# Kernel optimization log

Hardware: AMD Instinct MI355X
Metric: run time of the kernel (lower is better)

## Reference

```python
import jax, jax.numpy as jnp
import numpy as np

B = 32768
D_A, D_V, D_T = 512, 512, 768
D_KW, D_CTX, D_SPK = 256, 256, 128
H = 512
IN_A = D_V + D_T + D_KW + D_CTX + D_SPK  # 1920 = visual + other_dim (text+hidden+speaker)
IN_V = D_A + D_T + D_KW + D_CTX + D_SPK  # 1920


def _linear_params(key, din, dout):
    kw, kb = jax.random.split(key)
    bound = 1.0 / np.sqrt(din)
    W = jax.random.uniform(kw, (din, dout), jnp.float32, -bound, bound)
    b = jax.random.uniform(kb, (dout,), jnp.float32, -bound, bound)
    return W, b


def setup_inputs() -> dict:
    key = jax.random.key(0)
    ks = jax.random.split(key, 16)
    inp = {
        'audio': jax.random.normal(ks[0], (B, D_A), jnp.float32),
        'visual': jax.random.normal(ks[1], (B, D_V), jnp.float32),
        'text': jax.random.normal(ks[2], (B, D_T), jnp.float32),
        'keywords': jax.random.normal(ks[3], (B, D_KW), jnp.float32),
        'context': jax.random.normal(ks[4], (B, D_CTX), jnp.float32),
        'speaker_embed': jax.random.normal(ks[5], (B, D_SPK), jnp.float32),
    }
    # Masks restricted to dimensionally-consistent patterns: [0,1,1] or [1,0,1]
    r = jax.random.randint(ks[6], (B,), 0, 2)
    inp['modality_masks'] = jnp.stack([r, 1 - r, jnp.ones_like(r)], axis=1).astype(jnp.int32)
    # audio_imagination MLP params
    inp['aW1'], inp['ab1'] = _linear_params(ks[7], IN_A, H)
    inp['aW2'], inp['ab2'] = _linear_params(ks[8], H, H)
    inp['aW3'], inp['ab3'] = _linear_params(ks[9], H, D_A)
    # visual_imagination MLP params
    inp['vW1'], inp['vb1'] = _linear_params(ks[10], IN_V, H)
    inp['vW2'], inp['vb2'] = _linear_params(ks[11], H, H)
    inp['vW3'], inp['vb3'] = _linear_params(ks[12], H, D_V)
    return inp


def _mlp(x, W1, b1, W2, b2, W3, b3):
    h = jax.nn.relu(x @ W1 + b1)  # dropout is eval-mode identity
    h = jax.nn.relu(h @ W2 + b2)
    return h @ W3 + b3


def reference(audio, visual, text, keywords, context, speaker_embed, modality_masks,
              aW1, ab1, aW2, ab2, aW3, ab3,
              vW1, vb1, vW2, vb2, vW3, vb3):
    m = modality_masks.astype(audio.dtype)
    common = jnp.concatenate([keywords, context, speaker_embed], axis=-1)  # [B, 640]
    in_a = jnp.concatenate([visual, text, common], axis=-1)  # [B, IN_A]
    in_v = jnp.concatenate([audio, text, common], axis=-1)   # [B, IN_V]
    # Rows where the modality is present (mask==1) were omitted in the original
    # ragged stacking; here they are zeroed to keep a fixed [B, D] output.
    recon_audio = _mlp(in_a, aW1, ab1, aW2, ab2, aW3, ab3) * (1.0 - m[:, 0:1])
    recon_visual = _mlp(in_v, vW1, vb1, vW2, vb2, vW3, vb3) * (1.0 - m[:, 1:2])
    return recon_audio, recon_visual
```

## Files before the change

kernel.cpp:

```cpp
#include <hip/hip_runtime.h>
#include <stdint.h>

typedef __bf16 bf16;
typedef __bf16 bf16x8 __attribute__((ext_vector_type(8)));
typedef float  f32x4  __attribute__((ext_vector_type(4)));

#define NROWS 32768
#define HID   512
#define PADM  17408

__device__ __forceinline__ void gload_lds16(const void* g, void* l) {
  __builtin_amdgcn_global_load_lds(
      (const __attribute__((address_space(1))) void*)g,
      (__attribute__((address_space(3))) void*)l, 16, 0, 0);
}

__global__ void prep_transpose(const float* __restrict__ W, bf16* __restrict__ WT,
                               int K, int N) {
  __shared__ float t[32][33];
  int k0 = blockIdx.x * 32, n0 = blockIdx.y * 32;
  int tx = threadIdx.x, ty = threadIdx.y;
#pragma unroll
  for (int p = 0; p < 4; ++p)
    t[ty + p * 8][tx] = W[(size_t)(k0 + ty + p * 8) * N + n0 + tx];
  __syncthreads();
#pragma unroll
  for (int p = 0; p < 4; ++p) {
    int n = n0 + ty + p * 8;
    int k = k0 + tx;
    int ks = (k & ~63) | (((((k >> 3) & 7) ^ (n & 7))) << 3) | (k & 7);
    WT[(size_t)n * K + ks] = (bf16)t[tx][ty + p * 8];
  }
}

__global__ void count_rows(const int* __restrict__ masks, int* __restrict__ bcnt) {
  int i = blockIdx.x * 256 + threadIdx.x;
  int lane = threadIdx.x & 63, wv = threadIdx.x >> 6;
  unsigned long long vA = __ballot(masks[i * 3] == 0);
  __shared__ int c[4];
  if (lane == 0) c[wv] = __popcll(vA);
  __syncthreads();
  if (threadIdx.x == 0) bcnt[blockIdx.x] = c[0] + c[1] + c[2] + c[3];
}

__global__ void scan_blocks(const int* __restrict__ bcnt, int* __restrict__ baseA,
                            int* __restrict__ counts) {
  __shared__ int s[128];
  s[threadIdx.x] = bcnt[threadIdx.x];
  __syncthreads();
  if (threadIdx.x == 0) {
    int run = 0;
    for (int i = 0; i < 128; ++i) { int v = s[i]; s[i] = run; run += v; }
    counts[0] = run; counts[1] = NROWS - run;
  }
  __syncthreads();
  baseA[threadIdx.x] = s[threadIdx.x];
}

__global__ void write_idx(const int* __restrict__ masks, const int* __restrict__ baseA,
                          int* __restrict__ idxA, int* __restrict__ idxV) {
  int b = blockIdx.x, t = threadIdx.x, i = b * 256 + t;
  int lane = t & 63, wv = t >> 6;
  int r = masks[i * 3];
  unsigned long long vA = __ballot(r == 0);
  __shared__ int wc[4];
  if (lane == 0) wc[wv] = __popcll(vA);
  __syncthreads();
  int wA = 0;
#pragma unroll
  for (int w = 0; w < 4; ++w) if (w < wv) wA += wc[w];
  unsigned long long ltmask = (lane == 63) ? (~0ULL >> 1) : ((1ULL << lane) - 1);
  int posA = __popcll(vA & ltmask);
  int bA = baseA[b];
  if (r == 0) idxA[bA + wA + posA] = i;
  else        idxV[(256 * b - bA) + (64 * wv - wA) + (lane - posA)] = i;
}

template <int LAYER>
__global__ __launch_bounds__(256, 4) void mlp_gemm(
    const float* __restrict__ audio, const float* __restrict__ visual,
    const float* __restrict__ text,  const float* __restrict__ kwd,
    const float* __restrict__ ctx,   const float* __restrict__ spk,
    const bf16*  __restrict__ hin,
    const bf16*  __restrict__ WTa,   const bf16* __restrict__ WTv,
    const float* __restrict__ ba,    const float* __restrict__ bv,
    const int*   __restrict__ counts,
    const int*   __restrict__ idxA,  const int* __restrict__ idxV,
    bf16* __restrict__ hout, float* __restrict__ out) {
  constexpr int K = (LAYER == 1) ? 1920 : 512;
  constexpr int NT = K / 64;
  const int mlp = blockIdx.z;
  const int cnt = counts[mlp];
  const int mb = (blockIdx.x & 7) * 34 + (blockIdx.x >> 3);
  const int m0 = mb * 64;
  if (m0 >= cnt) return;
  const int n0 = blockIdx.y * 128;
  const bf16*  WT   = mlp ? WTv : WTa;
  const float* bias = mlp ? bv : ba;
  const int*   idx  = mlp ? idxV : idxA;

  __shared__ __attribute__((aligned(16))) bf16 sA[64 * 64];
  __shared__ __attribute__((aligned(16))) bf16 sB[128 * 64];

  const int t = threadIdx.x;
  const int lane = t & 63;
  const int wave = t >> 6;
  const int wm = (wave >> 1) * 32;
  const int wn = (wave & 1) * 64;

  int gidx[2];
  if constexpr (LAYER == 1) {
#pragma unroll
    for (int rep = 0; rep < 2; ++rep) {
      int row = (t + rep * 256) >> 3;
      int i = m0 + row;
      if (i >= cnt) i = cnt - 1;
      gidx[rep] = idx[i];
    }
  }

  auto B_ISSUE = [&](int k0) {
#pragma unroll
    for (int j = 0; j < 4; ++j) {
      int sbase = (wave * 4 + j) * 64;
      int slot = sbase + lane;
      int row = slot >> 3, wc = slot & 7;
      gload_lds16(WT + (size_t)(n0 + row) * K + k0 + wc * 8, &sB[sbase * 8]);
    }
  };
  auto A_ISSUE_LDS = [&](int k0) {
#pragma unroll
    for (int j = 0; j < 2; ++j) {
      int sbase = (wave * 2 + j) * 64;
      int slot = sbase + lane;
      int row = slot >> 3, wc = slot & 7;
      gload_lds16(hin + ((size_t)mlp * PADM + m0 + row) * HID + k0 + wc * 8,
                  &sA[sbase * 8]);
    }
  };

  const f32x4 fzero = {0.f, 0.f, 0.f, 0.f};
  f32x4 acc[2][4];
#pragma unroll
  for (int a = 0; a < 2; ++a)
#pragma unroll
    for (int b = 0; b < 4; ++b) acc[a][b] = fzero;

  for (int ti = 0; ti < NT; ++ti) {
    const int k0 = ti * 64;
    __syncthreads();
    B_ISSUE(k0);
    if constexpr (LAYER >= 2) {
      A_ISSUE_LDS(k0);
    } else {
      const float* seg; int soff, sstr;
      if (k0 < 512)       { seg = mlp ? audio : visual; soff = k0;        sstr = 512; }
      else if (k0 < 1280) { seg = text; soff = k0 - 512;  sstr = 768; }
      else if (k0 < 1536) { seg = kwd;  soff = k0 - 1280; sstr = 256; }
      else if (k0 < 1792) { seg = ctx;  soff = k0 - 1536; sstr = 256; }
      else                { seg = spk;  soff = k0 - 1792; sstr = 128; }
#pragma unroll
      for (int rep = 0; rep < 2; ++rep) {
        int slot = t + rep * 256;
        int row = slot >> 3, c = slot & 7;
        int wc = c ^ (row & 7);
        const float* src = seg + (size_t)gidx[rep] * sstr + soff + c * 8;
        f32x4 lo = *(const f32x4*)src;
        f32x4 hi = *(const f32x4*)(src + 4);
        bf16x8 v;
        v[0] = (bf16)lo[0]; v[1] = (bf16)lo[1]; v[2] = (bf16)lo[2]; v[3] = (bf16)lo[3];
        v[4] = (bf16)hi[0]; v[5] = (bf16)hi[1]; v[6] = (bf16)hi[2]; v[7] = (bf16)hi[3];
        *(bf16x8*)&sA[row * 64 + wc * 8] = v;
      }
    }
    __syncthreads();

    bf16x8 af[2][2], bfr[4][2];
#pragma unroll
    for (int mf = 0; mf < 2; ++mf)
#pragma unroll
      for (int kh = 0; kh < 2; ++kh) {
        int row = wm + mf * 16 + (lane & 15);
        int c = (lane >> 4) + kh * 4;
        af[mf][kh] = *(const bf16x8*)&sA[row * 64 + (c ^ (row & 7)) * 8];
      }
#pragma unroll
    for (int nf = 0; nf < 4; ++nf)
#pragma unroll
      for (int kh = 0; kh < 2; ++kh) {
        int row = wn + nf * 16 + (lane & 15);
        int c = (lane >> 4) + kh * 4;
        bfr[nf][kh] = *(const bf16x8*)&sB[row * 64 + (c ^ (row & 7)) * 8];
      }
#pragma unroll
    for (int mf = 0; mf < 2; ++mf)
#pragma unroll
      for (int nf = 0; nf < 4; ++nf)
#pragma unroll
        for (int kh = 0; kh < 2; ++kh)
          acc[mf][nf] = __builtin_amdgcn_mfma_f32_16x16x32_bf16(
              af[mf][kh], bfr[nf][kh], acc[mf][nf], 0, 0, 0);
  }

  const int r4 = (lane >> 4) * 4;
  const int cl = lane & 15;
#pragma unroll
  for (int mf = 0; mf < 2; ++mf) {
#pragma unroll
    for (int reg = 0; reg < 4; ++reg) {
      int lrow = wm + mf * 16 + r4 + reg;
      int grow = m0 + lrow;
      if (grow >= cnt) continue;
      if constexpr (LAYER < 3) {
#pragma unroll
        for (int nf = 0; nf < 4; ++nf) {
          int col = n0 + wn + nf * 16 + cl;
          float v = acc[mf][nf][reg] + bias[col];
          v = fmaxf(v, 0.f);
          int cs = (col & ~63) | (((((col >> 3) & 7) ^ (grow & 7))) << 3) | (col & 7);
          hout[((size_t)mlp * PADM + grow) * HID + cs] = (bf16)v;
        }
      } else {
        int g = idx[grow];
#pragma unroll
        for (int nf = 0; nf < 4; ++nf) {
          int col = n0 + wn + nf * 16 + cl;
          float v = acc[mf][nf][reg] + bias[col];
          out[((size_t)mlp * NROWS + g) * 512 + col] = v;
          out[((size_t)(1 - mlp) * NROWS + g) * 512 + col] = 0.f;
        }
      }
    }
  }
}

extern "C" void kernel_launch(void* const* d_in, const int* in_sizes, int n_in,
                              void* d_out, int out_size, void* d_ws, size_t ws_size,
                              hipStream_t stream) {
  (void)in_sizes; (void)n_in; (void)out_size;
  const float* audio  = (const float*)d_in[0];
  const float* visual = (const float*)d_in[1];
  const float* text   = (const float*)d_in[2];
  const float* kwd    = (const float*)d_in[3];
  const float* ctx    = (const float*)d_in[4];
  const float* spk    = (const float*)d_in[5];
  const int*   masks  = (const int*)d_in[6];
  const float* aW1 = (const float*)d_in[7];  const float* ab1 = (const float*)d_in[8];
  const float* aW2 = (const float*)d_in[9];  const float* ab2 = (const float*)d_in[10];
  const float* aW3 = (const float*)d_in[11]; const float* ab3 = (const float*)d_in[12];
  const float* vW1 = (const float*)d_in[13]; const float* vb1 = (const float*)d_in[14];
  const float* vW2 = (const float*)d_in[15]; const float* vb2 = (const float*)d_in[16];
  const float* vW3 = (const float*)d_in[17]; const float* vb3 = (const float*)d_in[18];
  float* out = (float*)d_out;

  char* w = (char*)d_ws;
  int* counts = (int*)w;
  int* bcnt   = (int*)(w + 256);
  int* baseA  = (int*)(w + 1024);
  int* idxA = (int*)(w + 4096);
  int* idxV = idxA + 32768;
  bf16* aW1t = (bf16*)(w + 4096 + 262144);
  bf16* vW1t = aW1t + 983040;
  bf16* aW2t = vW1t + 983040;
  bf16* vW2t = aW2t + 262144;
  bf16* aW3t = vW2t + 262144;
  bf16* vW3t = aW3t + 262144;
  bf16* h1 = vW3t + 262144;
  bf16* h2 = h1 + (size_t)2 * PADM * HID;
  (void)ws_size;

  count_rows<<<128, 256, 0, stream>>>(masks, bcnt);
  scan_blocks<<<1, 128, 0, stream>>>(bcnt, baseA, counts);
  write_idx<<<128, 256, 0, stream>>>(masks, baseA, idxA, idxV);

  dim3 tb(32, 8);
  prep_transpose<<<dim3(60, 16), tb, 0, stream>>>(aW1, aW1t, 1920, 512);
  prep_transpose<<<dim3(60, 16), tb, 0, stream>>>(vW1, vW1t, 1920, 512);
  prep_transpose<<<dim3(16, 16), tb, 0, stream>>>(aW2, aW2t, 512, 512);
  prep_transpose<<<dim3(16, 16), tb, 0, stream>>>(vW2, vW2t, 512, 512);
  prep_transpose<<<dim3(16, 16), tb, 0, stream>>>(aW3, aW3t, 512, 512);
  prep_transpose<<<dim3(16, 16), tb, 0, stream>>>(vW3, vW3t, 512, 512);

  dim3 gg(272, 4, 2);
  mlp_gemm<1><<<gg, 256, 0, stream>>>(audio, visual, text, kwd, ctx, spk, nullptr,
                                      aW1t, vW1t, ab1, vb1, counts, idxA, idxV, h1, nullptr);
  mlp_gemm<2><<<gg, 256, 0, stream>>>(audio, visual, text, kwd, ctx, spk, h1,
                                      aW2t, vW2t, ab2, vb2, counts, idxA, idxV, h2, nullptr);
  mlp_gemm<3><<<gg, 256, 0, stream>>>(audio, visual, text, kwd, ctx, spk, h2,
                                      aW3t, vW3t, ab3, vb3, counts, idxA, idxV, nullptr, out);
}
```

Baseline: 267.7 us.

## Use full-width 128x512 output tiles with 512-thread blocks per MLP

Each block now computes a 128-row by full 512-column tile with 8 waves, instead of a 64x128 tile. The MLP index moves from blockIdx.z into the XCD bits of blockIdx.x, and the grid shrinks to 272 one-dimensional blocks. This is meant to load (and, in layer 1, gather and convert from fp32) each activation row once rather than once per N tile, and to raise MFMA work per LDS fragment load. In exchange it uses 80KB of LDS and 128 accumulator registers per thread, so only one block fits per CU, which leaves few waves to hide the unpipelined global loads.

```diff
diff --git a/kernel.cpp b/kernel.cpp
--- a/kernel.cpp
+++ b/kernel.cpp
@@ -77,7 +77,7 @@
 }
 
 template <int LAYER>
-__global__ __launch_bounds__(256, 4) void mlp_gemm(
+__global__ __launch_bounds__(512, 1) void mlp_gemm(
     const float* __restrict__ audio, const float* __restrict__ visual,
     const float* __restrict__ text,  const float* __restrict__ kwd,
     const float* __restrict__ ctx,   const float* __restrict__ spk,
@@ -89,30 +89,33 @@
     bf16* __restrict__ hout, float* __restrict__ out) {
   constexpr int K = (LAYER == 1) ? 1920 : 512;
   constexpr int NT = K / 64;
-  const int mlp = blockIdx.z;
+  const int bx = blockIdx.x;
+  const int xcd = bx & 7;
+  const int mlp = xcd >> 2;
+  const int mb = (xcd & 3) * 34 + (bx >> 3);
+  const int m0 = mb * 128;
   const int cnt = counts[mlp];
-  const int mb = (blockIdx.x & 7) * 34 + (blockIdx.x >> 3);
-  const int m0 = mb * 64;
   if (m0 >= cnt) return;
-  const int n0 = blockIdx.y * 128;
   const bf16*  WT   = mlp ? WTv : WTa;
   const float* bias = mlp ? bv : ba;
   const int*   idx  = mlp ? idxV : idxA;
 
-  __shared__ __attribute__((aligned(16))) bf16 sA[64 * 64];
-  __shared__ __attribute__((aligned(16))) bf16 sB[128 * 64];
+  __shared__ __attribute__((aligned(16))) bf16 sA[128 * 64];
+  __shared__ __attribute__((aligned(16))) bf16 sB[512 * 64];
 
   const int t = threadIdx.x;
   const int lane = t & 63;
   const int wave = t >> 6;
-  const int wm = (wave >> 1) * 32;
-  const int wn = (wave & 1) * 64;
+  const int wm = (wave >> 2) * 64;
+  const int wn = (wave & 3) * 128;
+  const int cl = lane & 15;
+  const int qw = lane >> 4;
 
   int gidx[2];
   if constexpr (LAYER == 1) {
 #pragma unroll
     for (int rep = 0; rep < 2; ++rep) {
-      int row = (t + rep * 256) >> 3;
+      int row = (t + rep * 512) >> 3;
       int i = m0 + row;
       if (i >= cnt) i = cnt - 1;
       gidx[rep] = idx[i];
@@ -121,11 +124,11 @@
 
   auto B_ISSUE = [&](int k0) {
 #pragma unroll
-    for (int j = 0; j < 4; ++j) {
-      int sbase = (wave * 4 + j) * 64;
+    for (int j = 0; j < 8; ++j) {
+      int sbase = (wave * 8 + j) * 64;
       int slot = sbase + lane;
       int row = slot >> 3, wc = slot & 7;
-      gload_lds16(WT + (size_t)(n0 + row) * K + k0 + wc * 8, &sB[sbase * 8]);
+      gload_lds16(WT + (size_t)row * K + k0 + wc * 8, &sB[sbase * 8]);
     }
   };
   auto A_ISSUE_LDS = [&](int k0) {
@@ -140,11 +143,11 @@
   };
 
   const f32x4 fzero = {0.f, 0.f, 0.f, 0.f};
-  f32x4 acc[2][4];
-#pragma unroll
-  for (int a = 0; a < 2; ++a)
-#pragma unroll
-    for (int b = 0; b < 4; ++b) acc[a][b] = fzero;
+  f32x4 acc[4][8];
+#pragma unroll
+  for (int a = 0; a < 4; ++a)
+#pragma unroll
+    for (int b = 0; b < 8; ++b) acc[a][b] = fzero;
 
   for (int ti = 0; ti < NT; ++ti) {
     const int k0 = ti * 64;
@@ -161,7 +164,7 @@
       else                { seg = spk;  soff = k0 - 1792; sstr = 128; }
 #pragma unroll
       for (int rep = 0; rep < 2; ++rep) {
-        int slot = t + rep * 256;
+        int slot = t + rep * 512;
         int row = slot >> 3, c = slot & 7;
         int wc = c ^ (row & 7);
         const float* src = seg + (size_t)gidx[rep] * sstr + soff + c * 8;
@@ -175,37 +178,31 @@
     }
     __syncthreads();
 
-    bf16x8 af[2][2], bfr[4][2];
-#pragma unroll
-    for (int mf = 0; mf < 2; ++mf)
-#pragma unroll
-      for (int kh = 0; kh < 2; ++kh) {
-        int row = wm + mf * 16 + (lane & 15);
-        int c = (lane >> 4) + kh * 4;
-        af[mf][kh] = *(const bf16x8*)&sA[row * 64 + (c ^ (row & 7)) * 8];
-      }
-#pragma unroll
-    for (int nf = 0; nf < 4; ++nf)
-#pragma unroll
-      for (int kh = 0; kh < 2; ++kh) {
-        int row = wn + nf * 16 + (lane & 15);
-        int c = (lane >> 4) + kh * 4;
-        bfr[nf][kh] = *(const bf16x8*)&sB[row * 64 + (c ^ (row & 7)) * 8];
-      }
-#pragma unroll
-    for (int mf = 0; mf < 2; ++mf)
-#pragma unroll
-      for (int nf = 0; nf < 4; ++nf)
-#pragma unroll
-        for (int kh = 0; kh < 2; ++kh)
+#pragma unroll
+    for (int kh = 0; kh < 2; ++kh) {
+      bf16x8 af[4];
+#pragma unroll
+      for (int mf = 0; mf < 4; ++mf) {
+        int row = wm + mf * 16 + cl;
+        int c = qw + kh * 4;
+        af[mf] = *(const bf16x8*)&sA[row * 64 + ((c ^ (row & 7)) << 3)];
+      }
+#pragma unroll
+      for (int nf = 0; nf < 8; ++nf) {
+        int row = wn + nf * 16 + cl;
+        int c = qw + kh * 4;
+        bf16x8 bfr = *(const bf16x8*)&sB[row * 64 + ((c ^ (row & 7)) << 3)];
+#pragma unroll
+        for (int mf = 0; mf < 4; ++mf)
           acc[mf][nf] = __builtin_amdgcn_mfma_f32_16x16x32_bf16(
-              af[mf][kh], bfr[nf][kh], acc[mf][nf], 0, 0, 0);
-  }
-
-  const int r4 = (lane >> 4) * 4;
-  const int cl = lane & 15;
-#pragma unroll
-  for (int mf = 0; mf < 2; ++mf) {
+              af[mf], bfr, acc[mf][nf], 0, 0, 0);
+      }
+    }
+  }
+
+  const int r4 = qw * 4;
+#pragma unroll
+  for (int mf = 0; mf < 4; ++mf) {
 #pragma unroll
     for (int reg = 0; reg < 4; ++reg) {
       int lrow = wm + mf * 16 + r4 + reg;
@@ -213,8 +210,8 @@
       if (grow >= cnt) continue;
       if constexpr (LAYER < 3) {
 #pragma unroll
-        for (int nf = 0; nf < 4; ++nf) {
-          int col = n0 + wn + nf * 16 + cl;
+        for (int nf = 0; nf < 8; ++nf) {
+          int col = wn + nf * 16 + cl;
           float v = acc[mf][nf][reg] + bias[col];
           v = fmaxf(v, 0.f);
           int cs = (col & ~63) | (((((col >> 3) & 7) ^ (grow & 7))) << 3) | (col & 7);
@@ -223,8 +220,8 @@
       } else {
         int g = idx[grow];
 #pragma unroll
-        for (int nf = 0; nf < 4; ++nf) {
-          int col = n0 + wn + nf * 16 + cl;
+        for (int nf = 0; nf < 8; ++nf) {
+          int col = wn + nf * 16 + cl;
           float v = acc[mf][nf][reg] + bias[col];
           out[((size_t)mlp * NROWS + g) * 512 + col] = v;
           out[((size_t)(1 - mlp) * NROWS + g) * 512 + col] = 0.f;
@@ -281,11 +278,11 @@
   prep_transpose<<<dim3(16, 16), tb, 0, stream>>>(aW3, aW3t, 512, 512);
   prep_transpose<<<dim3(16, 16), tb, 0, stream>>>(vW3, vW3t, 512, 512);
 
-  dim3 gg(272, 4, 2);
-  mlp_gemm<1><<<gg, 256, 0, stream>>>(audio, visual, text, kwd, ctx, spk, nullptr,
+  dim3 gg(272);
+  mlp_gemm<1><<<gg, 512, 0, stream>>>(audio, visual, text, kwd, ctx, spk, nullptr,
                                       aW1t, vW1t, ab1, vb1, counts, idxA, idxV, h1, nullptr);
-  mlp_gemm<2><<<gg, 256, 0, stream>>>(audio, visual, text, kwd, ctx, spk, h1,
+  mlp_gemm<2><<<gg, 512, 0, stream>>>(audio, visual, text, kwd, ctx, spk, h1,
                                       aW2t, vW2t, ab2, vb2, counts, idxA, idxV, h2, nullptr);
-  mlp_gemm<3><<<gg, 256, 0, stream>>>(audio, visual, text, kwd, ctx, spk, h2,
+  mlp_gemm<3><<<gg, 512, 0, stream>>>(audio, visual, text, kwd, ctx, spk, h2,
                                       aW3t, vW3t, ab3, vb3, counts, idxA, idxV, nullptr, out);
 }
```

Result: slower. 345.1 us (+28.9%).
